# Kernel optimization log

Hardware: AMD Instinct MI355X
Metric: run time of the kernel (lower is better)

The kernel has to match this reference:

```python
import jax, jax.numpy as jnp
import numpy as np

N = 50000
E = 640000
IN_DIM = 23
HID = 128
NUM_CLASS = 12


def setup_inputs() -> dict:
    key = jax.random.key(0)
    ks = jax.random.split(key, 12)
    x = jax.random.normal(ks[0], (N, IN_DIM), dtype=jnp.float32)
    edge_index = jax.random.randint(ks[1], (2, E), 0, N, dtype=jnp.int32)

    def glorot(k, shape):
        fan_in, fan_out = shape
        lim = np.sqrt(6.0 / (fan_in + fan_out)).astype(np.float32)
        return jax.random.uniform(k, shape, jnp.float32, -lim, lim)

    W1 = glorot(ks[2], (IN_DIM, HID)); b1 = jnp.zeros((HID,), jnp.float32)
    W2 = glorot(ks[3], (HID, HID));    b2 = jnp.zeros((HID,), jnp.float32)
    W3 = glorot(ks[4], (HID, HID));    b3 = jnp.zeros((HID,), jnp.float32)
    Wc1 = glorot(ks[5], (HID, 64));    bc1 = jnp.zeros((64,), jnp.float32)
    Wc2 = glorot(ks[6], (64, NUM_CLASS)); bc2 = jnp.zeros((NUM_CLASS,), jnp.float32)
    return {"x": x, "edge_index": edge_index,
            "W1": W1, "b1": b1, "W2": W2, "b2": b2, "W3": W3, "b3": b3,
            "Wc1": Wc1, "bc1": bc1, "Wc2": Wc2, "bc2": bc2}


def _gcn_norm(edge_index, n_nodes):
    # add self loops, compute symmetric normalization D^-1/2 (A+I) D^-1/2
    loop = jnp.arange(n_nodes, dtype=edge_index.dtype)
    src = jnp.concatenate([edge_index[0], loop])
    dst = jnp.concatenate([edge_index[1], loop])
    deg = jax.ops.segment_sum(jnp.ones_like(dst, dtype=jnp.float32), dst,
                              num_segments=n_nodes)
    dinv = jax.lax.rsqrt(deg)  # deg >= 1 due to self loops
    norm = dinv[src] * dinv[dst]  # [E + N]
    return src, dst, norm


def _gcn_layer(h, W, b, src, dst, norm, n_nodes):
    h = h @ W                          # linear (bias applied after aggregation, per PyG)
    msg = h[src] * norm[:, None]       # gather + scale
    out = jax.ops.segment_sum(msg, dst, num_segments=n_nodes)  # scatter-add
    return out + b


def reference(x, edge_index, W1, b1, W2, b2, W3, b3, Wc1, bc1, Wc2, bc2):
    n = x.shape[0]
    src, dst, norm = _gcn_norm(edge_index, n)
    h = jnp.tanh(_gcn_layer(x, W1, b1, src, dst, norm, n))
    h = jnp.tanh(_gcn_layer(h, W2, b2, src, dst, norm, n))
    h = jnp.tanh(_gcn_layer(h, W3, b3, src, dst, norm, n))
    # dropout is identity in eval mode
    out = h @ Wc1 + bc1
    out = out @ Wc2 + bc2
    return out
```

## Files before the change

### kernel.cpp

```cpp
#include <hip/hip_runtime.h>
#include <math.h>

#define NN 50000
#define EE 640000
#define IND 23
#define HID 128
#define MIDD 64
#define NCLS 12
#define NB 49
#define QS 32766.0f
#define INVQS (1.0f / 32766.0f)

typedef short short8v __attribute__((ext_vector_type(8)));


__global__ void k_count(const int* __restrict__ dst, int* __restrict__ cnt, int e) {
    int i = blockIdx.x * blockDim.x + threadIdx.x;
    if (i < e) atomicAdd(&cnt[dst[i]], 1);
}

__global__ __launch_bounds__(256) void k_scan_local(const int* __restrict__ cnt,
                                                    int* __restrict__ row_ptr,
                                                    float* __restrict__ dinv,
                                                    int* __restrict__ sums) {
    __shared__ int wtot[4];
    const int tid = threadIdx.x;
    const int wid = tid >> 6, lane = tid & 63;
    const int base = blockIdx.x * 1024 + tid * 4;
    int v[4];
#pragma unroll
    for (int t = 0; t < 4; ++t) {
        int i = base + t;
        v[t] = (i < NN) ? cnt[i] : 0;
        if (i < NN) dinv[i] = rsqrtf((float)v[t] + 1.0f);
    }
    int slocal = v[0] + v[1] + v[2] + v[3];
    int val = slocal;
#pragma unroll
    for (int off = 1; off < 64; off <<= 1) {
        int t = __shfl_up(val, off, 64);
        if (lane >= off) val += t;
    }
    if (lane == 63) wtot[wid] = val;
    __syncthreads();
    int woff = 0;
#pragma unroll
    for (int w = 0; w < 4; ++w) woff += (w < wid) ? wtot[w] : 0;
    int run = woff + val - slocal;
#pragma unroll
    for (int t = 0; t < 4; ++t) {
        int i = base + t;
        if (i < NN) row_ptr[i] = run;
        run += v[t];
    }
    if (tid == 255) sums[blockIdx.x] = woff + val;
}

__global__ void k_scan_sums(const int* __restrict__ sums, int* __restrict__ offs,
                            int* __restrict__ row_ptr) {
    const int lane = threadIdx.x;
    int v = (lane < NB) ? sums[lane] : 0;
    int val = v;
#pragma unroll
    for (int off = 1; off < 64; off <<= 1) {
        int t = __shfl_up(val, off, 64);
        if (lane >= off) val += t;
    }
    if (lane < NB) offs[lane] = val - v;
    if (lane == NB - 1) row_ptr[NN] = val;
}

__global__ __launch_bounds__(256) void k_scan_apply(int* __restrict__ row_ptr,
                                                    const int* __restrict__ offs,
                                                    int* __restrict__ cursor) {
    const int base = blockIdx.x * 1024 + threadIdx.x * 4;
    const int o = offs[blockIdx.x];
#pragma unroll
    for (int t = 0; t < 4; ++t) {
        int i = base + t;
        if (i < NN) {
            int rp = row_ptr[i] + o;
            row_ptr[i] = rp;
            cursor[i] = rp;
        }
    }
}

__global__ void k_fill(const int* __restrict__ src, const int* __restrict__ dst,
                       int* __restrict__ cursor, const float* __restrict__ dinv,
                       int2* __restrict__ e_sn, int e) {
    int i = blockIdx.x * blockDim.x + threadIdx.x;
    if (i < e) {
        int s = src[i];
        int d = dst[i];
        float w = dinv[s];
        int pos = atomicAdd(&cursor[d], 1);
        e_sn[pos] = make_int2(s, __float_as_int(w));
    }
}

__global__ __launch_bounds__(256) void k_pad(const float* __restrict__ x,
                                             const float* __restrict__ dinv,
                                             float* __restrict__ xp) {
    int i = blockIdx.x * 256 + threadIdx.x;
    int node = i >> 5, f = i & 31;
    xp[i] = (f < IND) ? x[node * IND + f] * dinv[node] : 0.f;
}

__global__ void k_wcc(const float* __restrict__ Wc1, const float* __restrict__ bc1,
                      const float* __restrict__ Wc2, const float* __restrict__ bc2,
                      float* __restrict__ Wcc, float* __restrict__ bcc) {
    int t = blockIdx.x * 256 + threadIdx.x;
    if (t < HID * NCLS) {
        int k = t / NCLS, c = t % NCLS;
        float s = 0.f;
#pragma unroll 8
        for (int j = 0; j < MIDD; ++j) s += Wc1[k * MIDD + j] * Wc2[j * NCLS + c];
        Wcc[t] = s;
    }
    if (t < NCLS) {
        float s = bc2[t];
#pragma unroll 8
        for (int j = 0; j < MIDD; ++j) s += bc1[j] * Wc2[j * NCLS + t];
        bcc[t] = s;
    }
}

__global__ __launch_bounds__(256) void k_l1(const float* __restrict__ xp,
                                            const float* __restrict__ W1,
                                            const float* __restrict__ b1,
                                            const int* __restrict__ row_ptr,
                                            const int2* __restrict__ e_sn,
                                            const float* __restrict__ dinv,
                                            short* __restrict__ outq) {
    const int tid = threadIdx.x;
    const int i = blockIdx.x * 4 + (tid >> 6);
    const int lane = tid & 63;
    const int slot = lane >> 3;
    const int f = lane & 7;
    const float4* xp4 = (const float4*)xp;
    const int beg = row_ptr[i];
    const int deg = row_ptr[i + 1] - beg;
    float4 acc = make_float4(0.f, 0.f, 0.f, 0.f);
    for (int base = 0; base < deg; base += 64) {
        const int cnt = min(64, deg - base);
        int s_l = 0;
        if (lane < cnt) s_l = e_sn[beg + base + lane].x;
        int e = 0;
        for (; e + 8 <= cnt; e += 8) {
            int s = __shfl(s_l, e + slot, 64);
            float4 v = xp4[s * 8 + f];
            acc.x += v.x; acc.y += v.y; acc.z += v.z; acc.w += v.w;
        }
        if (e < cnt) {
            int s = __shfl(s_l, e + slot, 64);
            if (e + slot < cnt) {
                float4 v = xp4[s * 8 + f];
                acc.x += v.x; acc.y += v.y; acc.z += v.z; acc.w += v.w;
            }
        }
    }
#pragma unroll
    for (int off = 32; off >= 8; off >>= 1) {
        acc.x += __shfl_down(acc.x, off, 64);
        acc.y += __shfl_down(acc.y, off, 64);
        acc.z += __shfl_down(acc.z, off, 64);
        acc.w += __shfl_down(acc.w, off, 64);
    }
    const float di = dinv[i];
    if (lane < 8) {
        float4 v = xp4[i * 8 + lane];
        acc.x = (acc.x + v.x) * di; acc.y = (acc.y + v.y) * di;
        acc.z = (acc.z + v.z) * di; acc.w = (acc.w + v.w) * di;
    }
    float a0 = b1[lane], a1 = b1[lane + 64];
#pragma unroll
    for (int k = 0; k < IND; ++k) {
        float comp = ((k & 3) == 0) ? acc.x : ((k & 3) == 1) ? acc.y
                   : ((k & 3) == 2) ? acc.z : acc.w;
        float xk = __shfl(comp, k >> 2, 64);
        a0 += xk * W1[k * HID + lane];
        a1 += xk * W1[k * HID + lane + 64];
    }
    outq[i * HID + lane]      = (short)__float2int_rn(tanhf(a0) * QS);
    outq[i * HID + lane + 64] = (short)__float2int_rn(tanhf(a1) * QS);
}

__global__ __launch_bounds__(256) void k_aggq(const short* __restrict__ hq,
                                              const int* __restrict__ row_ptr,
                                              const int2* __restrict__ e_sn,
                                              const float* __restrict__ dinv,
                                              float* __restrict__ aggf) {
    const int tid = threadIdx.x;
    const int i = blockIdx.x * 4 + (tid >> 6);
    const int lane = tid & 63;
    const int slot = lane >> 4;
    const int f = lane & 15;
    const short8v* h8 = (const short8v*)hq;
    const int beg = row_ptr[i];
    const int deg = row_ptr[i + 1] - beg;
    float facc[8];
#pragma unroll
    for (int t = 0; t < 8; ++t) facc[t] = 0.f;
    for (int base = 0; base < deg; base += 64) {
        const int cnt = min(64, deg - base);
        int s_l = 0; float n_l = 0.f;
        if (lane < cnt) {
            int2 sn = e_sn[beg + base + lane];
            s_l = sn.x;
            n_l = __int_as_float(sn.y);
        }
        int e = 0;
#pragma unroll 4
        for (; e + 4 <= cnt; e += 4) {
            int s = __shfl(s_l, e + slot, 64);
            float nr = __shfl(n_l, e + slot, 64);
            short8v v = h8[s * 16 + f];
#pragma unroll
            for (int t = 0; t < 8; ++t) facc[t] += (float)v[t] * nr;
        }
        if (e < cnt) {
            int s = __shfl(s_l, e + slot, 64);
            float nr = __shfl(n_l, e + slot, 64);
            if (e + slot < cnt) {
                short8v v = h8[s * 16 + f];
#pragma unroll
                for (int t = 0; t < 8; ++t) facc[t] += (float)v[t] * nr;
            }
        }
    }
#pragma unroll
    for (int off = 32; off >= 16; off >>= 1)
#pragma unroll
        for (int t = 0; t < 8; ++t) facc[t] += __shfl_down(facc[t], off, 64);
    if (lane < 16) {
        const float di = dinv[i];
        const float sc = di * INVQS;
        short8v v = h8[i * 16 + lane];
        float4 o0, o1;
        o0.x = (facc[0] + di * (float)v[0]) * sc;
        o0.y = (facc[1] + di * (float)v[1]) * sc;
        o0.z = (facc[2] + di * (float)v[2]) * sc;
        o0.w = (facc[3] + di * (float)v[3]) * sc;
        o1.x = (facc[4] + di * (float)v[4]) * sc;
        o1.y = (facc[5] + di * (float)v[5]) * sc;
        o1.z = (facc[6] + di * (float)v[6]) * sc;
        o1.w = (facc[7] + di * (float)v[7]) * sc;
        ((float4*)aggf)[i * 32 + lane * 2]     = o0;
        ((float4*)aggf)[i * 32 + lane * 2 + 1] = o1;
    }
}

__global__ __launch_bounds__(256) void k_gemmT(const float* __restrict__ hin,
                                               const float* __restrict__ W,
                                               const float* __restrict__ bias,
                                               short* __restrict__ qout,
                                               const float* __restrict__ Wcc,
                                               const float* __restrict__ bcc,
                                               float* __restrict__ outp) {
    __shared__ float Smem[64 * 36 + 32 * 128];
    float* Hs = Smem;
    float* Ws = Smem + 64 * 36;
    const int tid = threadIdx.x;
    const int b0 = blockIdx.x * 64;
    const int ng = tid >> 4;
    const int cg = tid & 15;
    const float4* hin4 = (const float4*)hin;
    const float4* W4 = (const float4*)W;

    float acc[4][8];
#pragma unroll
    for (int m = 0; m < 4; ++m)
#pragma unroll
        for (int c = 0; c < 8; ++c) acc[m][c] = 0.f;

    for (int ks = 0; ks < HID; ks += 32) {
#pragma unroll
        for (int t = 0; t < 2; ++t) {
            int id = t * 256 + tid;
            int row = id >> 3;
            int k4 = id & 7;
            int node = b0 + row;
            float4 v = make_float4(0.f, 0.f, 0.f, 0.f);
            if (node < NN) v = hin4[node * 32 + (ks >> 2) + k4];
            *(float4*)&Hs[row * 36 + k4 * 4] = v;
        }
#pragma unroll
        for (int t = 0; t < 4; ++t) {
            int id = t * 256 + tid;
            int row = id >> 5;
            int c4 = id & 31;
            *(float4*)&Ws[row * 128 + c4 * 4] = W4[(ks + row) * 32 + c4];
        }
        __syncthreads();
#pragma unroll
        for (int kk = 0; kk < 32; kk += 4) {
            float4 h4[4];
#pragma unroll
            for (int m = 0; m < 4; ++m)
                h4[m] = *(float4*)&Hs[(ng * 4 + m) * 36 + kk];
#pragma unroll
            for (int j = 0; j < 4; ++j) {
                float4 w0 = *(float4*)&Ws[(kk + j) * 128 + cg * 8];
                float4 w1 = *(float4*)&Ws[(kk + j) * 128 + cg * 8 + 4];
#pragma unroll
                for (int m = 0; m < 4; ++m) {
                    float hv = (j == 0) ? h4[m].x : (j == 1) ? h4[m].y
                             : (j == 2) ? h4[m].z : h4[m].w;
                    acc[m][0] += hv * w0.x; acc[m][1] += hv * w0.y;
                    acc[m][2] += hv * w0.z; acc[m][3] += hv * w0.w;
                    acc[m][4] += hv * w1.x; acc[m][5] += hv * w1.y;
                    acc[m][6] += hv * w1.z; acc[m][7] += hv * w1.w;
                }
            }
        }
        __syncthreads();
    }
    const float4* b4 = (const float4*)bias;
    float4 bb0 = b4[cg * 2], bb1 = b4[cg * 2 + 1];
#pragma unroll
    for (int m = 0; m < 4; ++m) {
        acc[m][0] = tanhf(acc[m][0] + bb0.x);
        acc[m][1] = tanhf(acc[m][1] + bb0.y);
        acc[m][2] = tanhf(acc[m][2] + bb0.z);
        acc[m][3] = tanhf(acc[m][3] + bb0.w);
        acc[m][4] = tanhf(acc[m][4] + bb1.x);
        acc[m][5] = tanhf(acc[m][5] + bb1.y);
        acc[m][6] = tanhf(acc[m][6] + bb1.z);
        acc[m][7] = tanhf(acc[m][7] + bb1.w);
    }

    if (outp == nullptr) {
#pragma unroll
        for (int m = 0; m < 4; ++m) {
            int node = b0 + ng * 4 + m;
            if (node < NN && qout) {
                short8v qv;
                qv[0] = (short)__float2int_rn(acc[m][0] * QS);
                qv[1] = (short)__float2int_rn(acc[m][1] * QS);
                qv[2] = (short)__float2int_rn(acc[m][2] * QS);
                qv[3] = (short)__float2int_rn(acc[m][3] * QS);
                qv[4] = (short)__float2int_rn(acc[m][4] * QS);
                qv[5] = (short)__float2int_rn(acc[m][5] * QS);
                qv[6] = (short)__float2int_rn(acc[m][6] * QS);
                qv[7] = (short)__float2int_rn(acc[m][7] * QS);
                ((short8v*)qout)[node * 16 + cg] = qv;
            }
        }
        return;
    }

    float* H3 = Smem;
    float* WccS = Smem + 32 * 132;
    float* bccS = WccS + HID * NCLS;
    for (int t = tid; t < HID * NCLS; t += 256) WccS[t] = Wcc[t];
    if (tid < NCLS) bccS[tid] = bcc[tid];
#pragma unroll
    for (int h = 0; h < 2; ++h) {
        if (h) __syncthreads();
        if ((ng >> 3) == h) {
            int r = (ng - h * 8) * 4;
#pragma unroll
            for (int m = 0; m < 4; ++m) {
                *(float4*)&H3[(r + m) * 132 + cg * 8] =
                    make_float4(acc[m][0], acc[m][1], acc[m][2], acc[m][3]);
                *(float4*)&H3[(r + m) * 132 + cg * 8 + 4] =
                    make_float4(acc[m][4], acc[m][5], acc[m][6], acc[m][7]);
            }
        }
        __syncthreads();
        const int n32 = tid >> 3, oct = tid & 7;
        float a0 = 0.f, a1 = 0.f, a2 = 0.f, a3 = 0.f, a4 = 0.f, a5 = 0.f,
              a6 = 0.f, a7 = 0.f, a8 = 0.f, a9 = 0.f, a10 = 0.f, a11 = 0.f;
#pragma unroll
        for (int kk = 0; kk < 16; ++kk) {
            int k = kk * 8 + oct;
            float hv = H3[n32 * 132 + k];
            const float4* wr = (const float4*)&WccS[k * NCLS];
            float4 wa = wr[0], wb = wr[1], wc = wr[2];
            a0 += hv * wa.x; a1 += hv * wa.y; a2  += hv * wa.z; a3  += hv * wa.w;
            a4 += hv * wb.x; a5 += hv * wb.y; a6  += hv * wb.z; a7  += hv * wb.w;
            a8 += hv * wc.x; a9 += hv * wc.y; a10 += hv * wc.z; a11 += hv * wc.w;
        }
#pragma unroll
        for (int off = 4; off; off >>= 1) {
            a0 += __shfl_down(a0, off, 64);   a1 += __shfl_down(a1, off, 64);
            a2 += __shfl_down(a2, off, 64);   a3 += __shfl_down(a3, off, 64);
            a4 += __shfl_down(a4, off, 64);   a5 += __shfl_down(a5, off, 64);
            a6 += __shfl_down(a6, off, 64);   a7 += __shfl_down(a7, off, 64);
            a8 += __shfl_down(a8, off, 64);   a9 += __shfl_down(a9, off, 64);
            a10 += __shfl_down(a10, off, 64); a11 += __shfl_down(a11, off, 64);
        }
        int node = b0 + h * 32 + n32;
        if (oct == 0 && node < NN) {
            float4* op = (float4*)&outp[node * NCLS];
            op[0] = make_float4(a0 + bccS[0], a1 + bccS[1], a2 + bccS[2], a3 + bccS[3]);
            op[1] = make_float4(a4 + bccS[4], a5 + bccS[5], a6 + bccS[6], a7 + bccS[7]);
            op[2] = make_float4(a8 + bccS[8], a9 + bccS[9], a10 + bccS[10], a11 + bccS[11]);
        }
    }
}


extern "C" void kernel_launch(void* const* d_in, const int* in_sizes, int n_in,
                              void* d_out, int out_size, void* d_ws, size_t ws_size,
                              hipStream_t stream) {
    const float* x    = (const float*)d_in[0];
    const int*   edge = (const int*)d_in[1];
    const int*   src  = edge;
    const int*   dst  = edge + EE;
    const float* W1  = (const float*)d_in[2];  const float* b1  = (const float*)d_in[3];
    const float* W2  = (const float*)d_in[4];  const float* b2  = (const float*)d_in[5];
    const float* W3  = (const float*)d_in[6];  const float* b3  = (const float*)d_in[7];
    const float* Wc1 = (const float*)d_in[8];  const float* bc1 = (const float*)d_in[9];
    const float* Wc2 = (const float*)d_in[10]; const float* bc2 = (const float*)d_in[11];
    float* outp = (float*)d_out;

    char* p = (char*)d_ws;
    int*   cnt     = (int*)p;   p += 200064;
    int*   row_ptr = (int*)p;   p += 200064;
    float* dinv    = (float*)p; p += 200064;
    int*   sums    = (int*)p;   p += 256;
    int*   offs    = (int*)p;   p += 256;
    int2*  e_sn    = (int2*)p;  p += (size_t)EE * 8;
    float* xp      = (float*)p; p += (size_t)NN * 32 * 4;
    short* q       = (short*)p; p += (size_t)NN * HID * 2;
    float* aggf    = (float*)p; p += (size_t)NN * HID * 4;
    float* Wcc     = (float*)p; p += HID * NCLS * 4;
    float* bcc     = (float*)p; p += 256;

    hipMemsetAsync(cnt, 0, (size_t)NN * 4, stream);
    k_wcc       <<<(HID * NCLS + 255) / 256, 256, 0, stream>>>(Wc1, bc1, Wc2, bc2, Wcc, bcc);
    k_count     <<<(EE + 255) / 256, 256, 0, stream>>>(dst, cnt, EE);
    k_scan_local<<<NB, 256, 0, stream>>>(cnt, row_ptr, dinv, sums);
    k_scan_sums <<<1, 64, 0, stream>>>(sums, offs, row_ptr);
    k_scan_apply<<<NB, 256, 0, stream>>>(row_ptr, offs, cnt);
    k_fill      <<<(EE + 255) / 256, 256, 0, stream>>>(src, dst, cnt, dinv, e_sn, EE);
    k_pad       <<<(NN * 32) / 256, 256, 0, stream>>>(x, dinv, xp);

    k_l1  <<<NN / 4, 256, 0, stream>>>(xp, W1, b1, row_ptr, e_sn, dinv, q);
    k_aggq <<<NN / 4, 256, 0, stream>>>(q, row_ptr, e_sn, dinv, aggf);
    k_gemmT<<<(NN + 63) / 64, 256, 0, stream>>>(aggf, W2, b2, q, nullptr, nullptr, nullptr);
    k_aggq <<<NN / 4, 256, 0, stream>>>(q, row_ptr, e_sn, dinv, aggf);
    k_gemmT<<<(NN + 63) / 64, 256, 0, stream>>>(aggf, W3, b3, nullptr, Wcc, bcc, outp);
}
```

Baseline: 331.0 us.

## Replace FP32 SIMT GEMMs with split-bf16 MFMA GEMMs for layers two and three

Each 128x128 layer GEMM now runs on MFMA bf16 16x16x32 instructions instead of scalar FP32 FMAs through LDS tiles. Accuracy is kept close to FP32 by splitting activations and weights into hi and lo bf16 parts and issuing three MFMAs (hi*hi, hi*lo, lo*hi). A new pre-pass kernel splits and re-lays-out W2 and W3 into an MFMA-friendly fragment order. The fused classifier head is rewritten to reduce over the MFMA output layout with shuffles. This triples the MFMA count, drops LDS staging of activations, and adds one small extra launch.

```diff
diff --git a/kernel.cpp b/kernel.cpp
--- a/kernel.cpp
+++ b/kernel.cpp
@@ -12,6 +12,16 @@
 #define INVQS (1.0f / 32766.0f)
 
 typedef short short8v __attribute__((ext_vector_type(8)));
+typedef float f32x4 __attribute__((ext_vector_type(4)));
+
+__device__ __forceinline__ short f2bf(float f) {
+    unsigned u = __float_as_uint(f);
+    unsigned r = (u + 0x7FFFu + ((u >> 16) & 1u)) >> 16;
+    return (short)r;
+}
+__device__ __forceinline__ float bf2f(short s) {
+    return __uint_as_float(((unsigned)(unsigned short)s) << 16);
+}
 
 
 __global__ void k_count(const int* __restrict__ dst, int* __restrict__ cnt, int e) {
@@ -124,6 +134,23 @@
         for (int j = 0; j < MIDD; ++j) s += bc1[j] * Wc2[j * NCLS + t];
         bcc[t] = s;
     }
+}
+
+__global__ void k_wsplit(const float* __restrict__ Wa, const float* __restrict__ Wb,
+                         short* __restrict__ hiA, short* __restrict__ loA,
+                         short* __restrict__ hiB, short* __restrict__ loB) {
+    int i = blockIdx.x * 256 + threadIdx.x;
+    const float* W = (blockIdx.y == 0) ? Wa : Wb;
+    short* hi = (blockIdx.y == 0) ? hiA : hiB;
+    short* lo = (blockIdx.y == 0) ? loA : loB;
+    int k = i >> 7, c = i & 127;
+    float w = W[i];
+    short h = f2bf(w);
+    short l = f2bf(w - bf2f(h));
+    int t = k >> 5, g = (k >> 3) & 3, j = k & 7;
+    int idx = ((t * 4 + g) * 128 + c) * 8 + j;
+    hi[idx] = h;
+    lo[idx] = l;
 }
 
 __global__ __launch_bounds__(256) void k_l1(const float* __restrict__ xp,
@@ -251,152 +278,135 @@
     }
 }
 
-__global__ __launch_bounds__(256) void k_gemmT(const float* __restrict__ hin,
-                                               const float* __restrict__ W,
-                                               const float* __restrict__ bias,
-                                               short* __restrict__ qout,
-                                               const float* __restrict__ Wcc,
-                                               const float* __restrict__ bcc,
-                                               float* __restrict__ outp) {
-    __shared__ float Smem[64 * 36 + 32 * 128];
-    float* Hs = Smem;
-    float* Ws = Smem + 64 * 36;
+__device__ __forceinline__ void gemm_core(const float* __restrict__ hin,
+                                          const short8v* __restrict__ whi8,
+                                          const short8v* __restrict__ wlo8,
+                                          int row, bool rv, int g, int c16,
+                                          f32x4 acc[8]) {
+#pragma unroll
+    for (int t = 0; t < 4; ++t) {
+        float4 a0 = make_float4(0.f, 0.f, 0.f, 0.f), a1 = a0;
+        if (rv) {
+            const float4* hp = (const float4*)&hin[row * HID + t * 32 + g * 8];
+            a0 = hp[0]; a1 = hp[1];
+        }
+        float av[8];
+        av[0] = a0.x; av[1] = a0.y; av[2] = a0.z; av[3] = a0.w;
+        av[4] = a1.x; av[5] = a1.y; av[6] = a1.z; av[7] = a1.w;
+        short8v ahi, alo;
+#pragma unroll
+        for (int j = 0; j < 8; ++j) {
+            short h = f2bf(av[j]);
+            ahi[j] = h;
+            alo[j] = f2bf(av[j] - bf2f(h));
+        }
+        const int wb = (t * 4 + g) * 128 + c16;
+#pragma unroll
+        for (int n = 0; n < 8; ++n) {
+            short8v bh = whi8[wb + n * 16];
+            short8v bl = wlo8[wb + n * 16];
+            acc[n] = __builtin_amdgcn_mfma_f32_16x16x32_bf16(ahi, bh, acc[n], 0, 0, 0);
+            acc[n] = __builtin_amdgcn_mfma_f32_16x16x32_bf16(ahi, bl, acc[n], 0, 0, 0);
+            acc[n] = __builtin_amdgcn_mfma_f32_16x16x32_bf16(alo, bh, acc[n], 0, 0, 0);
+        }
+    }
+}
+
+__global__ __launch_bounds__(256) void k_gemm_q(const float* __restrict__ hin,
+                                                const short* __restrict__ whi,
+                                                const short* __restrict__ wlo,
+                                                const float* __restrict__ bias,
+                                                short* __restrict__ qout) {
     const int tid = threadIdx.x;
-    const int b0 = blockIdx.x * 64;
-    const int ng = tid >> 4;
-    const int cg = tid & 15;
-    const float4* hin4 = (const float4*)hin;
-    const float4* W4 = (const float4*)W;
-
-    float acc[4][8];
-#pragma unroll
-    for (int m = 0; m < 4; ++m)
-#pragma unroll
-        for (int c = 0; c < 8; ++c) acc[m][c] = 0.f;
-
-    for (int ks = 0; ks < HID; ks += 32) {
-#pragma unroll
-        for (int t = 0; t < 2; ++t) {
-            int id = t * 256 + tid;
-            int row = id >> 3;
-            int k4 = id & 7;
-            int node = b0 + row;
-            float4 v = make_float4(0.f, 0.f, 0.f, 0.f);
-            if (node < NN) v = hin4[node * 32 + (ks >> 2) + k4];
-            *(float4*)&Hs[row * 36 + k4 * 4] = v;
-        }
-#pragma unroll
-        for (int t = 0; t < 4; ++t) {
-            int id = t * 256 + tid;
-            int row = id >> 5;
-            int c4 = id & 31;
-            *(float4*)&Ws[row * 128 + c4 * 4] = W4[(ks + row) * 32 + c4];
-        }
-        __syncthreads();
-#pragma unroll
-        for (int kk = 0; kk < 32; kk += 4) {
-            float4 h4[4];
-#pragma unroll
-            for (int m = 0; m < 4; ++m)
-                h4[m] = *(float4*)&Hs[(ng * 4 + m) * 36 + kk];
-#pragma unroll
-            for (int j = 0; j < 4; ++j) {
-                float4 w0 = *(float4*)&Ws[(kk + j) * 128 + cg * 8];
-                float4 w1 = *(float4*)&Ws[(kk + j) * 128 + cg * 8 + 4];
-#pragma unroll
-                for (int m = 0; m < 4; ++m) {
-                    float hv = (j == 0) ? h4[m].x : (j == 1) ? h4[m].y
-                             : (j == 2) ? h4[m].z : h4[m].w;
-                    acc[m][0] += hv * w0.x; acc[m][1] += hv * w0.y;
-                    acc[m][2] += hv * w0.z; acc[m][3] += hv * w0.w;
-                    acc[m][4] += hv * w1.x; acc[m][5] += hv * w1.y;
-                    acc[m][6] += hv * w1.z; acc[m][7] += hv * w1.w;
-                }
+    const int lane = tid & 63, w = tid >> 6;
+    const int g = lane >> 4, c16 = lane & 15;
+    const int rbase = blockIdx.x * 64 + w * 16;
+    f32x4 acc[8];
+#pragma unroll
+    for (int n = 0; n < 8; ++n) acc[n] = f32x4{0.f, 0.f, 0.f, 0.f};
+    gemm_core(hin, (const short8v*)whi, (const short8v*)wlo,
+              rbase + c16, (rbase + c16) < NN, g, c16, acc);
+#pragma unroll
+    for (int n = 0; n < 8; ++n) {
+        const float bb = bias[n * 16 + c16];
+#pragma unroll
+        for (int r = 0; r < 4; ++r) {
+            int nd = rbase + 4 * g + r;
+            if (nd < NN) {
+                float v = tanhf(acc[n][r] + bb);
+                qout[nd * HID + n * 16 + c16] = (short)__float2int_rn(v * QS);
             }
         }
-        __syncthreads();
-    }
-    const float4* b4 = (const float4*)bias;
-    float4 bb0 = b4[cg * 2], bb1 = b4[cg * 2 + 1];
-#pragma unroll
-    for (int m = 0; m < 4; ++m) {
-        acc[m][0] = tanhf(acc[m][0] + bb0.x);
-        acc[m][1] = tanhf(acc[m][1] + bb0.y);
-        acc[m][2] = tanhf(acc[m][2] + bb0.z);
-        acc[m][3] = tanhf(acc[m][3] + bb0.w);
-        acc[m][4] = tanhf(acc[m][4] + bb1.x);
-        acc[m][5] = tanhf(acc[m][5] + bb1.y);
-        acc[m][6] = tanhf(acc[m][6] + bb1.z);
-        acc[m][7] = tanhf(acc[m][7] + bb1.w);
-    }
-
-    if (outp == nullptr) {
-#pragma unroll
-        for (int m = 0; m < 4; ++m) {
-            int node = b0 + ng * 4 + m;
-            if (node < NN && qout) {
-                short8v qv;
-                qv[0] = (short)__float2int_rn(acc[m][0] * QS);
-                qv[1] = (short)__float2int_rn(acc[m][1] * QS);
-                qv[2] = (short)__float2int_rn(acc[m][2] * QS);
-                qv[3] = (short)__float2int_rn(acc[m][3] * QS);
-                qv[4] = (short)__float2int_rn(acc[m][4] * QS);
-                qv[5] = (short)__float2int_rn(acc[m][5] * QS);
-                qv[6] = (short)__float2int_rn(acc[m][6] * QS);
-                qv[7] = (short)__float2int_rn(acc[m][7] * QS);
-                ((short8v*)qout)[node * 16 + cg] = qv;
+    }
+}
+
+__global__ __launch_bounds__(256) void k_gemm_head(const float* __restrict__ hin,
+                                                   const short* __restrict__ whi,
+                                                   const short* __restrict__ wlo,
+                                                   const float* __restrict__ bias,
+                                                   const float* __restrict__ Wcc,
+                                                   const float* __restrict__ bcc,
+                                                   float* __restrict__ outp) {
+    __shared__ float WccS[HID * NCLS + 16];
+    const int tid = threadIdx.x;
+    const int lane = tid & 63, w = tid >> 6;
+    const int g = lane >> 4, c16 = lane & 15;
+    const int rbase = blockIdx.x * 64 + w * 16;
+    for (int t = tid; t < HID * NCLS; t += 256) WccS[t] = Wcc[t];
+    if (tid < NCLS) WccS[HID * NCLS + tid] = bcc[tid];
+    __syncthreads();
+    f32x4 acc[8];
+#pragma unroll
+    for (int n = 0; n < 8; ++n) acc[n] = f32x4{0.f, 0.f, 0.f, 0.f};
+    gemm_core(hin, (const short8v*)whi, (const short8v*)wlo,
+              rbase + c16, (rbase + c16) < NN, g, c16, acc);
+    float part[4][12];
+#pragma unroll
+    for (int r = 0; r < 4; ++r)
+#pragma unroll
+        for (int c = 0; c < 12; ++c) part[r][c] = 0.f;
+#pragma unroll
+    for (int n = 0; n < 8; ++n) {
+        const float bb = bias[n * 16 + c16];
+        const float4* wr = (const float4*)&WccS[(n * 16 + c16) * NCLS];
+        float4 wa = wr[0], wb = wr[1], wc = wr[2];
+#pragma unroll
+        for (int r = 0; r < 4; ++r) {
+            float v = tanhf(acc[n][r] + bb);
+            part[r][0]  += v * wa.x; part[r][1]  += v * wa.y;
+            part[r][2]  += v * wa.z; part[r][3]  += v * wa.w;
+            part[r][4]  += v * wb.x; part[r][5]  += v * wb.y;
+            part[r][6]  += v * wb.z; part[r][7]  += v * wb.w;
+            part[r][8]  += v * wc.x; part[r][9]  += v * wc.y;
+            part[r][10] += v * wc.z; part[r][11] += v * wc.w;
+        }
+    }
+#pragma unroll
+    for (int off = 8; off; off >>= 1)
+#pragma unroll
+        for (int r = 0; r < 4; ++r)
+#pragma unroll
+            for (int c = 0; c < 12; ++c)
+                part[r][c] += __shfl_down(part[r][c], off, 64);
+    if (c16 == 0) {
+#pragma unroll
+        for (int r = 0; r < 4; ++r) {
+            int nd = rbase + 4 * g + r;
+            if (nd < NN) {
+                float4* op = (float4*)&outp[nd * NCLS];
+                op[0] = make_float4(part[r][0] + WccS[HID * NCLS + 0],
+                                    part[r][1] + WccS[HID * NCLS + 1],
+                                    part[r][2] + WccS[HID * NCLS + 2],
+                                    part[r][3] + WccS[HID * NCLS + 3]);
+                op[1] = make_float4(part[r][4] + WccS[HID * NCLS + 4],
+                                    part[r][5] + WccS[HID * NCLS + 5],
+                                    part[r][6] + WccS[HID * NCLS + 6],
+                                    part[r][7] + WccS[HID * NCLS + 7]);
+                op[2] = make_float4(part[r][8] + WccS[HID * NCLS + 8],
+                                    part[r][9] + WccS[HID * NCLS + 9],
+                                    part[r][10] + WccS[HID * NCLS + 10],
+                                    part[r][11] + WccS[HID * NCLS + 11]);
             }
-        }
-        return;
-    }
-
-    float* H3 = Smem;
-    float* WccS = Smem + 32 * 132;
-    float* bccS = WccS + HID * NCLS;
-    for (int t = tid; t < HID * NCLS; t += 256) WccS[t] = Wcc[t];
-    if (tid < NCLS) bccS[tid] = bcc[tid];
-#pragma unroll
-    for (int h = 0; h < 2; ++h) {
-        if (h) __syncthreads();
-        if ((ng >> 3) == h) {
-            int r = (ng - h * 8) * 4;
-#pragma unroll
-            for (int m = 0; m < 4; ++m) {
-                *(float4*)&H3[(r + m) * 132 + cg * 8] =
-                    make_float4(acc[m][0], acc[m][1], acc[m][2], acc[m][3]);
-                *(float4*)&H3[(r + m) * 132 + cg * 8 + 4] =
-                    make_float4(acc[m][4], acc[m][5], acc[m][6], acc[m][7]);
-            }
-        }
-        __syncthreads();
-        const int n32 = tid >> 3, oct = tid & 7;
-        float a0 = 0.f, a1 = 0.f, a2 = 0.f, a3 = 0.f, a4 = 0.f, a5 = 0.f,
-              a6 = 0.f, a7 = 0.f, a8 = 0.f, a9 = 0.f, a10 = 0.f, a11 = 0.f;
-#pragma unroll
-        for (int kk = 0; kk < 16; ++kk) {
-            int k = kk * 8 + oct;
-            float hv = H3[n32 * 132 + k];
-            const float4* wr = (const float4*)&WccS[k * NCLS];
-            float4 wa = wr[0], wb = wr[1], wc = wr[2];
-            a0 += hv * wa.x; a1 += hv * wa.y; a2  += hv * wa.z; a3  += hv * wa.w;
-            a4 += hv * wb.x; a5 += hv * wb.y; a6  += hv * wb.z; a7  += hv * wb.w;
-            a8 += hv * wc.x; a9 += hv * wc.y; a10 += hv * wc.z; a11 += hv * wc.w;
-        }
-#pragma unroll
-        for (int off = 4; off; off >>= 1) {
-            a0 += __shfl_down(a0, off, 64);   a1 += __shfl_down(a1, off, 64);
-            a2 += __shfl_down(a2, off, 64);   a3 += __shfl_down(a3, off, 64);
-            a4 += __shfl_down(a4, off, 64);   a5 += __shfl_down(a5, off, 64);
-            a6 += __shfl_down(a6, off, 64);   a7 += __shfl_down(a7, off, 64);
-            a8 += __shfl_down(a8, off, 64);   a9 += __shfl_down(a9, off, 64);
-            a10 += __shfl_down(a10, off, 64); a11 += __shfl_down(a11, off, 64);
-        }
-        int node = b0 + h * 32 + n32;
-        if (oct == 0 && node < NN) {
-            float4* op = (float4*)&outp[node * NCLS];
-            op[0] = make_float4(a0 + bccS[0], a1 + bccS[1], a2 + bccS[2], a3 + bccS[3]);
-            op[1] = make_float4(a4 + bccS[4], a5 + bccS[5], a6 + bccS[6], a7 + bccS[7]);
-            op[2] = make_float4(a8 + bccS[8], a9 + bccS[9], a10 + bccS[10], a11 + bccS[11]);
         }
     }
 }
@@ -428,9 +438,14 @@
     float* aggf    = (float*)p; p += (size_t)NN * HID * 4;
     float* Wcc     = (float*)p; p += HID * NCLS * 4;
     float* bcc     = (float*)p; p += 256;
+    short* w2hi    = (short*)p; p += 32768;
+    short* w2lo    = (short*)p; p += 32768;
+    short* w3hi    = (short*)p; p += 32768;
+    short* w3lo    = (short*)p; p += 32768;
 
     hipMemsetAsync(cnt, 0, (size_t)NN * 4, stream);
     k_wcc       <<<(HID * NCLS + 255) / 256, 256, 0, stream>>>(Wc1, bc1, Wc2, bc2, Wcc, bcc);
+    k_wsplit    <<<dim3(64, 2), 256, 0, stream>>>(W2, W3, w2hi, w2lo, w3hi, w3lo);
     k_count     <<<(EE + 255) / 256, 256, 0, stream>>>(dst, cnt, EE);
     k_scan_local<<<NB, 256, 0, stream>>>(cnt, row_ptr, dinv, sums);
     k_scan_sums <<<1, 64, 0, stream>>>(sums, offs, row_ptr);
@@ -439,8 +454,8 @@
     k_pad       <<<(NN * 32) / 256, 256, 0, stream>>>(x, dinv, xp);
 
     k_l1  <<<NN / 4, 256, 0, stream>>>(xp, W1, b1, row_ptr, e_sn, dinv, q);
-    k_aggq <<<NN / 4, 256, 0, stream>>>(q, row_ptr, e_sn, dinv, aggf);
-    k_gemmT<<<(NN + 63) / 64, 256, 0, stream>>>(aggf, W2, b2, q, nullptr, nullptr, nullptr);
-    k_aggq <<<NN / 4, 256, 0, stream>>>(q, row_ptr, e_sn, dinv, aggf);
-    k_gemmT<<<(NN + 63) / 64, 256, 0, stream>>>(aggf, W3, b3, nullptr, Wcc, bcc, outp);
-}
+    k_aggq     <<<NN / 4, 256, 0, stream>>>(q, row_ptr, e_sn, dinv, aggf);
+    k_gemm_q   <<<(NN + 63) / 64, 256, 0, stream>>>(aggf, w2hi, w2lo, b2, q);
+    k_aggq     <<<NN / 4, 256, 0, stream>>>(q, row_ptr, e_sn, dinv, aggf);
+    k_gemm_head<<<(NN + 63) / 64, 256, 0, stream>>>(aggf, w3hi, w3lo, b3, Wcc, bcc, outp);
+}
```

Result: faster. 304.5 us (-8.0%).
